# Kernel tuning notes

Measured on AMD Instinct MI355X. Metric: run time of the kernel, lower is better.

The kernel has to match this reference:

```python
import jax, jax.numpy as jnp
import numpy as np

NEG_SLOPE = 0.1  # LeakyReLU alpha from __init__
EPS = 1e-5


def setup_inputs() -> dict:
    key = jax.random.key(0)
    k1, k2, k3, k4, k5 = jax.random.split(key, 5)
    N, E, DIN, DOUT = 10000, 160000, 1024, 1024
    x = jax.random.normal(k1, (N, DIN), dtype=jnp.float32)
    W = jax.random.normal(k2, (DIN, DOUT), dtype=jnp.float32) * 0.02  # xavier-ish gain
    a = jax.random.normal(k3, (1, 2 * DOUT), dtype=jnp.float32) * 0.02
    src = jax.random.randint(k4, (E,), 0, N, dtype=jnp.int64)  # edge rows i
    dst = jax.random.randint(k5, (E,), 0, N, dtype=jnp.int64)  # edge cols j
    return {"x": x, "W": W, "a": a, "src": src, "dst": dst}


def reference(x, W, a, src, dst):
    N = x.shape[0]
    d = W.shape[1]
    h = x @ W                                   # [N, d]
    # a @ cat(h_src, h_dst)^T == (h @ a_l)[src] + (h @ a_r)[dst]
    a_l, a_r = a[0, :d], a[0, d:]
    al = h @ a_l                                # [N]
    ar = h @ a_r                                # [N]
    e = jnp.exp(-jax.nn.leaky_relu(al[src] + ar[dst], negative_slope=NEG_SLOPE))  # [E]
    # sparse rowsum: A @ ones  ->  segment_sum of e over rows
    rowsum = jax.ops.segment_sum(e, src, num_segments=N)          # [N]
    # sparse aggregate: A @ h  (dropout = identity in eval mode)
    h_prime = jax.ops.segment_sum(e[:, None] * h[dst], src, num_segments=N)  # [N, d]
    h_prime = h_prime / (rowsum[:, None] + EPS)
    return jax.nn.elu(h_prime)  # concat=True branch
```

## Files before the change

### kernel.cpp

```cpp
#include <hip/hip_runtime.h>
#include <hip/hip_bf16.h>
#include <stdint.h>
#include <math.h>

#define DK 1024
#define DN 1024
#define CAP 64

typedef __attribute__((ext_vector_type(8))) short bf16x8;
typedef __attribute__((ext_vector_type(4))) float f32x4;
typedef __attribute__((ext_vector_type(8))) unsigned short u16x8;

__device__ __forceinline__ unsigned short f2bf(float f) {
  union { float f; uint32_t u; } v; v.f = f;
  uint32_t r = v.u + 0x7FFFu + ((v.u >> 16) & 1u);
  return (unsigned short)(r >> 16);
}
__device__ __forceinline__ float bf2f(unsigned short b) {
  union { uint32_t u; float f; } v; v.u = ((uint32_t)b) << 16; return v.f;
}

__device__ __forceinline__ void gload_lds16(const void* g, void* l) {
  __builtin_amdgcn_global_load_lds((const __attribute__((address_space(1))) unsigned int*)g,
                                   (__attribute__((address_space(3))) unsigned int*)l,
                                   16, 0, 0);
}

__device__ __forceinline__ void block_reduce2(float& pl, float& pr) {
#pragma unroll
  for (int off = 32; off >= 1; off >>= 1) {
    pl += __shfl_down(pl, off);
    pr += __shfl_down(pr, off);
  }
  __shared__ float sl[4], sr[4];
  int w = threadIdx.x >> 6, lane = threadIdx.x & 63;
  if (lane == 0) { sl[w] = pl; sr[w] = pr; }
  __syncthreads();
  if (threadIdx.x == 0) {
    pl = sl[0] + sl[1] + sl[2] + sl[3];
    pr = sr[0] + sr[1] + sr[2] + sr[3];
  }
}

__global__ __launch_bounds__(256) void wvec_kernel(const float* __restrict__ W,
                                                   const float* __restrict__ a,
                                                   float* __restrict__ wl,
                                                   float* __restrict__ wr,
                                                   int* __restrict__ cnt, int M) {
  int idx = blockIdx.x * 256 + threadIdx.x;
  if (idx < M) cnt[idx] = 0;
  int k = blockIdx.x;
  int tid = threadIdx.x;
  float4 wv = ((const float4*)(W + (size_t)k * DN))[tid];
  float4 l4 = ((const float4*)a)[tid];
  float4 r4 = ((const float4*)(a + DN))[tid];
  float pl = wv.x * l4.x + wv.y * l4.y + wv.z * l4.z + wv.w * l4.w;
  float pr = wv.x * r4.x + wv.y * r4.y + wv.z * r4.z + wv.w * r4.w;
  block_reduce2(pl, pr);
  if (tid == 0) { wl[k] = pl; wr[k] = pr; }
}

__global__ __launch_bounds__(256) void prep_kernel(const float* __restrict__ x,
                                                   unsigned short* __restrict__ xb,
                                                   const float* __restrict__ W,
                                                   unsigned short* __restrict__ Wt,
                                                   const float* __restrict__ wl,
                                                   const float* __restrict__ wr,
                                                   float* __restrict__ al,
                                                   float* __restrict__ ar,
                                                   int M) {
  if ((int)blockIdx.x < M) {
    int row = blockIdx.x;
    int tid = threadIdx.x;
    float4 v = ((const float4*)(x + (size_t)row * DK))[tid];
    ushort4 o;
    o.x = f2bf(v.x); o.y = f2bf(v.y); o.z = f2bf(v.z); o.w = f2bf(v.w);
    ((ushort4*)(xb + (size_t)row * DK))[tid] = o;
    float4 l4 = ((const float4*)wl)[tid];
    float4 r4 = ((const float4*)wr)[tid];
    float pl = v.x * l4.x + v.y * l4.y + v.z * l4.z + v.w * l4.w;
    float pr = v.x * r4.x + v.y * r4.y + v.z * r4.z + v.w * r4.w;
    block_reduce2(pl, pr);
    if (tid == 0) { al[row] = pl; ar[row] = pr; }
  } else {
    __shared__ float t[32][33];
    int bid = blockIdx.x - M;
    int tx = threadIdx.x & 31, ty = threadIdx.x >> 5;
    int bk = (bid & 31) * 32, bn = (bid >> 5) * 32;
#pragma unroll
    for (int rr = 0; rr < 4; ++rr) {
      int row = ty + rr * 8;
      t[row][tx] = W[(size_t)(bk + row) * DN + bn + tx];
    }
    __syncthreads();
#pragma unroll
    for (int rr = 0; rr < 4; ++rr) {
      int row = ty + rr * 8;
      Wt[(size_t)(bn + row) * DK + bk + tx] = f2bf(t[tx][row]);
    }
  }
}

__global__ __launch_bounds__(256) void gemm_kernel(const unsigned short* __restrict__ A,
                                                   const unsigned short* __restrict__ Bt,
                                                   unsigned short* __restrict__ Hb,
                                                   int M) {
  __shared__ unsigned short As[128 * 32];
  __shared__ unsigned short Bs[128 * 32];
  const int tid = threadIdx.x;
  const int w = tid >> 6, lane = tid & 63;
  const int r = lane & 15, q = lane >> 4;
  const int m0 = blockIdx.x * 128, n0 = blockIdx.y * 128;
  const int wr = (w >> 1) * 64, wc = (w & 1) * 64;

  const int c0 = w * 64 + lane;
  const int rowA0 = c0 >> 2, g0 = c0 & 3;
  const int rowA1 = rowA0 + 64;
  int gr0 = m0 + rowA0; if (gr0 >= M) gr0 = M - 1;
  int gr1 = m0 + rowA1; if (gr1 >= M) gr1 = M - 1;
  const unsigned short* gA0 = A + (size_t)gr0 * DK + g0 * 8;
  const unsigned short* gA1 = A + (size_t)gr1 * DK + g0 * 8;
  const unsigned short* gB0 = Bt + (size_t)(n0 + rowA0) * DK + g0 * 8;
  const unsigned short* gB1 = Bt + (size_t)(n0 + rowA1) * DK + g0 * 8;
  unsigned short* lA0 = As + w * 512;
  unsigned short* lA1 = As + 2048 + w * 512;
  unsigned short* lB0 = Bs + w * 512;
  unsigned short* lB1 = Bs + 2048 + w * 512;

  const f32x4 zero = {0.f, 0.f, 0.f, 0.f};
  f32x4 acc[4][4];
#pragma unroll
  for (int i = 0; i < 4; ++i)
#pragma unroll
    for (int j = 0; j < 4; ++j) acc[i][j] = zero;

  for (int k0 = 0; k0 < DK; k0 += 32) {
    gload_lds16(gA0, lA0);
    gload_lds16(gA1, lA1);
    gload_lds16(gB0, lB0);
    gload_lds16(gB1, lB1);
    gA0 += 32; gA1 += 32; gB0 += 32; gB1 += 32;
    __syncthreads();

    bf16x8 af[4], bfr[4];
#pragma unroll
    for (int i = 0; i < 4; ++i)
      af[i] = *(const bf16x8*)&As[(wr + i * 16 + r) * 32 + q * 8];
#pragma unroll
    for (int j = 0; j < 4; ++j)
      bfr[j] = *(const bf16x8*)&Bs[(wc + j * 16 + r) * 32 + q * 8];
#pragma unroll
    for (int i = 0; i < 4; ++i)
#pragma unroll
      for (int j = 0; j < 4; ++j)
        acc[i][j] = __builtin_amdgcn_mfma_f32_16x16x32_bf16(af[i], bfr[j], acc[i][j], 0, 0, 0);
    __syncthreads();
  }

#pragma unroll
  for (int i = 0; i < 4; ++i) {
#pragma unroll
    for (int reg = 0; reg < 4; ++reg) {
      int m = m0 + wr + i * 16 + q * 4 + reg;
      if (m < M) {
#pragma unroll
        for (int j = 0; j < 4; ++j) {
          int n = n0 + wc + j * 16 + r;
          Hb[(size_t)m * DN + n] = f2bf(acc[i][j][reg]);
        }
      }
    }
  }
}

__global__ __launch_bounds__(256) void edge_kernel(const int* __restrict__ src,
                                                   const int* __restrict__ dst,
                                                   const float* __restrict__ al,
                                                   const float* __restrict__ ar,
                                                   int* __restrict__ cnt,
                                                   int* __restrict__ bdst,
                                                   float* __restrict__ be, int E) {
  int i = blockIdx.x * 256 + threadIdx.x;
  if (i < E) {
    int s = src[i], d = dst[i];
    float v = al[s] + ar[d];
    float lr = v > 0.f ? v : 0.1f * v;
    float e = expf(-lr);
    int pos = atomicAdd(&cnt[s], 1);
    if (pos < CAP) {
      bdst[(s << 6) + pos] = d;
      be[(s << 6) + pos] = e;
    }
  }
}

__device__ __forceinline__ void agg_batch16(const int* __restrict__ bdst,
                                            const float* __restrict__ be,
                                            const unsigned short* __restrict__ Hc,
                                            int base, int p, int n,
                                            float (&acc)[8], float& rs) {
  int d[16]; float e[16];
#pragma unroll
  for (int u = 0; u < 4; ++u) {
    int4 d4 = *(const int4*)(bdst + base + p + 4 * u);
    float4 e4 = *(const float4*)(be + base + p + 4 * u);
    d[4 * u + 0] = d4.x; d[4 * u + 1] = d4.y; d[4 * u + 2] = d4.z; d[4 * u + 3] = d4.w;
    e[4 * u + 0] = e4.x; e[4 * u + 1] = e4.y; e[4 * u + 2] = e4.z; e[4 * u + 3] = e4.w;
  }
#pragma unroll
  for (int j = 0; j < 16; ++j) {
    bool valid = (p + j) < n;
    d[j] = valid ? d[j] : 0;
    e[j] = valid ? e[j] : 0.f;
  }
  u16x8 hv[16];
#pragma unroll
  for (int j = 0; j < 16; ++j)
    hv[j] = *(const u16x8*)(Hc + (size_t)d[j] * DN);
#pragma unroll
  for (int j = 0; j < 16; ++j) {
    float ej = e[j];
    rs += ej;
#pragma unroll
    for (int c = 0; c < 8; ++c)
      acc[c] += ej * bf2f(hv[j][c]);
  }
}

__global__ __launch_bounds__(256) void aggregate_kernel(const int* __restrict__ cnt,
                                                        const int* __restrict__ bdst,
                                                        const float* __restrict__ be,
                                                        const unsigned short* __restrict__ Hb,
                                                        float* __restrict__ out, int M) {
  int row = (blockIdx.x << 1) + (threadIdx.x >> 7);
  if (row >= M) return;
  int t = threadIdx.x & 127;
  int n = cnt[row]; if (n > CAP) n = CAP;
  int base = row << 6;
  size_t coff = (size_t)t * 8;
  const unsigned short* Hc = Hb + coff;
  float acc[8] = {0.f, 0.f, 0.f, 0.f, 0.f, 0.f, 0.f, 0.f};
  float rs = 0.f;

  agg_batch16(bdst, be, Hc, base, 0, n, acc, rs);
  if (n > 16)
    agg_batch16(bdst, be, Hc, base, 16, n, acc, rs);
  if (n > 32) {
    for (int p = 32; p < n; ++p) {
      int dd = bdst[base + p];
      float ee = be[base + p];
      rs += ee;
      u16x8 hvv = *(const u16x8*)(Hc + (size_t)dd * DN);
#pragma unroll
      for (int c = 0; c < 8; ++c)
        acc[c] += ee * bf2f(hvv[c]);
    }
  }

  float inv = 1.f / (rs + 1e-5f);
  f32x4 lo, hi;
#pragma unroll
  for (int c = 0; c < 4; ++c) {
    float v = acc[c] * inv;
    lo[c] = v > 0.f ? v : (expf(v) - 1.f);
  }
#pragma unroll
  for (int c = 0; c < 4; ++c) {
    float v = acc[c + 4] * inv;
    hi[c] = v > 0.f ? v : (expf(v) - 1.f);
  }
  f32x4* op = (f32x4*)(out + (size_t)row * DN + coff);
  __builtin_nontemporal_store(lo, op);
  __builtin_nontemporal_store(hi, op + 1);
}

extern "C" void kernel_launch(void* const* d_in, const int* in_sizes, int n_in,
                              void* d_out, int out_size, void* d_ws, size_t ws_size,
                              hipStream_t stream) {
  const float* x = (const float*)d_in[0];
  const float* W = (const float*)d_in[1];
  const float* a = (const float*)d_in[2];
  const int* src = (const int*)d_in[3];
  const int* dst = (const int*)d_in[4];
  float* out = (float*)d_out;
  const int M = in_sizes[0] / DK;
  const int E = in_sizes[3];

  size_t off = 0;
  auto alloc = [&](size_t bytes) -> void* {
    void* p = (char*)d_ws + off;
    off += (bytes + 255) & ~(size_t)255;
    return p;
  };
  unsigned short* xb   = (unsigned short*)alloc((size_t)M * DK * 2);
  unsigned short* Wt   = (unsigned short*)alloc((size_t)DK * DN * 2);
  unsigned short* Hb   = (unsigned short*)alloc((size_t)M * DN * 2);
  float*          al   = (float*)alloc((size_t)M * 4);
  float*          ar   = (float*)alloc((size_t)M * 4);
  float*          wl   = (float*)alloc((size_t)DK * 4);
  float*          wr   = (float*)alloc((size_t)DK * 4);
  int*            cnt  = (int*)alloc((size_t)M * 4);
  int*            bdst = (int*)alloc((size_t)M * CAP * 4);
  float*          be   = (float*)alloc((size_t)M * CAP * 4);

  wvec_kernel<<<DK, 256, 0, stream>>>(W, a, wl, wr, cnt, M);
  prep_kernel<<<M + (DK / 32) * (DN / 32), 256, 0, stream>>>(x, xb, W, Wt, wl, wr, al, ar, M);
  gemm_kernel<<<dim3((M + 127) / 128, DN / 128), 256, 0, stream>>>(xb, Wt, Hb, M);
  edge_kernel<<<(E + 255) / 256, 256, 0, stream>>>(src, dst, al, ar, cnt, bdst, be, E);
  aggregate_kernel<<<(M + 1) / 2, 256, 0, stream>>>(cnt, bdst, be, Hb, out, M);
}
```

Baseline: 194.0 us.

## Double-buffer GEMM LDS tiles to overlap global loads with MFMA

Doubles the shared-memory A/B tiles and prefetches the next K-slice into the alternate buffer while MFMAs run on the current one, dropping one barrier per iteration. This hides global-to-LDS load latency behind compute. It doubles LDS use per block (32KB), which can lower occupancy. Correctness relies on the barrier at the end of each step plus the implicit vmcnt wait before the next reads.

```diff
diff --git a/kernel.cpp b/kernel.cpp
--- a/kernel.cpp
+++ b/kernel.cpp
@@ -105,8 +105,8 @@
                                                    const unsigned short* __restrict__ Bt,
                                                    unsigned short* __restrict__ Hb,
                                                    int M) {
-  __shared__ unsigned short As[128 * 32];
-  __shared__ unsigned short Bs[128 * 32];
+  __shared__ unsigned short As[2][128 * 32];
+  __shared__ unsigned short Bs[2][128 * 32];
   const int tid = threadIdx.x;
   const int w = tid >> 6, lane = tid & 63;
   const int r = lane & 15, q = lane >> 4;
@@ -122,10 +122,8 @@
   const unsigned short* gA1 = A + (size_t)gr1 * DK + g0 * 8;
   const unsigned short* gB0 = Bt + (size_t)(n0 + rowA0) * DK + g0 * 8;
   const unsigned short* gB1 = Bt + (size_t)(n0 + rowA1) * DK + g0 * 8;
-  unsigned short* lA0 = As + w * 512;
-  unsigned short* lA1 = As + 2048 + w * 512;
-  unsigned short* lB0 = Bs + w * 512;
-  unsigned short* lB1 = Bs + 2048 + w * 512;
+  const int l0 = w * 512;
+  const int l1 = 2048 + w * 512;
 
   const f32x4 zero = {0.f, 0.f, 0.f, 0.f};
   f32x4 acc[4][4];
@@ -134,26 +132,39 @@
 #pragma unroll
     for (int j = 0; j < 4; ++j) acc[i][j] = zero;
 
-  for (int k0 = 0; k0 < DK; k0 += 32) {
-    gload_lds16(gA0, lA0);
-    gload_lds16(gA1, lA1);
-    gload_lds16(gB0, lB0);
-    gload_lds16(gB1, lB1);
-    gA0 += 32; gA1 += 32; gB0 += 32; gB1 += 32;
-    __syncthreads();
-
+  gload_lds16(gA0, &As[0][l0]);
+  gload_lds16(gA1, &As[0][l1]);
+  gload_lds16(gB0, &Bs[0][l0]);
+  gload_lds16(gB1, &Bs[0][l1]);
+  gA0 += 32; gA1 += 32; gB0 += 32; gB1 += 32;
+  __syncthreads();
+
+  for (int step = 0; step < 32; ++step) {
+    const int cur = step & 1;
+    if (step < 31) {
+      const int nxt = cur ^ 1;
+      gload_lds16(gA0, &As[nxt][l0]);
+      gload_lds16(gA1, &As[nxt][l1]);
+      gload_lds16(gB0, &Bs[nxt][l0]);
+      gload_lds16(gB1, &Bs[nxt][l1]);
+      gA0 += 32; gA1 += 32; gB0 += 32; gB1 += 32;
+    }
+
+    const unsigned short* Ab = &As[cur][0];
+    const unsigned short* Bb = &Bs[cur][0];
     bf16x8 af[4], bfr[4];
 #pragma unroll
     for (int i = 0; i < 4; ++i)
-      af[i] = *(const bf16x8*)&As[(wr + i * 16 + r) * 32 + q * 8];
+      af[i] = *(const bf16x8*)&Ab[(wr + i * 16 + r) * 32 + q * 8];
 #pragma unroll
     for (int j = 0; j < 4; ++j)
-      bfr[j] = *(const bf16x8*)&Bs[(wc + j * 16 + r) * 32 + q * 8];
+      bfr[j] = *(const bf16x8*)&Bb[(wc + j * 16 + r) * 32 + q * 8];
 #pragma unroll
     for (int i = 0; i < 4; ++i)
 #pragma unroll
       for (int j = 0; j < 4; ++j)
         acc[i][j] = __builtin_amdgcn_mfma_f32_16x16x32_bf16(af[i], bfr[j], acc[i][j], 0, 0, 0);
+
     __syncthreads();
   }
 
```

New measurement: 198.7 us. +2.4%, slower.

## Fuse attention projections into GEMM epilogue and drop wvec kernel

Applied to the files above, without the earlier changes.

The separate W·a precompute kernel and the per-row dot products in the prep kernel are removed. al and ar are now computed in the GEMM epilogue from the fp32 accumulators, using shuffle reductions and atomicAdd into buffers that the prep kernel zeroes. The aggregate kernel is also split into two launches over row halves. This saves one launch and the block reductions, but adds atomics and changes summation order. The split aggregate adds a launch and has no clear benefit.

```diff
diff --git a/kernel.cpp b/kernel.cpp
--- a/kernel.cpp
+++ b/kernel.cpp
@@ -26,49 +26,16 @@
                                    16, 0, 0);
 }
 
-__device__ __forceinline__ void block_reduce2(float& pl, float& pr) {
-#pragma unroll
-  for (int off = 32; off >= 1; off >>= 1) {
-    pl += __shfl_down(pl, off);
-    pr += __shfl_down(pr, off);
-  }
-  __shared__ float sl[4], sr[4];
-  int w = threadIdx.x >> 6, lane = threadIdx.x & 63;
-  if (lane == 0) { sl[w] = pl; sr[w] = pr; }
-  __syncthreads();
-  if (threadIdx.x == 0) {
-    pl = sl[0] + sl[1] + sl[2] + sl[3];
-    pr = sr[0] + sr[1] + sr[2] + sr[3];
-  }
-}
-
-__global__ __launch_bounds__(256) void wvec_kernel(const float* __restrict__ W,
-                                                   const float* __restrict__ a,
-                                                   float* __restrict__ wl,
-                                                   float* __restrict__ wr,
-                                                   int* __restrict__ cnt, int M) {
-  int idx = blockIdx.x * 256 + threadIdx.x;
-  if (idx < M) cnt[idx] = 0;
-  int k = blockIdx.x;
-  int tid = threadIdx.x;
-  float4 wv = ((const float4*)(W + (size_t)k * DN))[tid];
-  float4 l4 = ((const float4*)a)[tid];
-  float4 r4 = ((const float4*)(a + DN))[tid];
-  float pl = wv.x * l4.x + wv.y * l4.y + wv.z * l4.z + wv.w * l4.w;
-  float pr = wv.x * r4.x + wv.y * r4.y + wv.z * r4.z + wv.w * r4.w;
-  block_reduce2(pl, pr);
-  if (tid == 0) { wl[k] = pl; wr[k] = pr; }
-}
-
 __global__ __launch_bounds__(256) void prep_kernel(const float* __restrict__ x,
                                                    unsigned short* __restrict__ xb,
                                                    const float* __restrict__ W,
                                                    unsigned short* __restrict__ Wt,
-                                                   const float* __restrict__ wl,
-                                                   const float* __restrict__ wr,
                                                    float* __restrict__ al,
                                                    float* __restrict__ ar,
+                                                   int* __restrict__ cnt,
                                                    int M) {
+  int g = blockIdx.x * 256 + threadIdx.x;
+  if (g < M) { al[g] = 0.f; ar[g] = 0.f; cnt[g] = 0; }
   if ((int)blockIdx.x < M) {
     int row = blockIdx.x;
     int tid = threadIdx.x;
@@ -76,12 +43,6 @@
     ushort4 o;
     o.x = f2bf(v.x); o.y = f2bf(v.y); o.z = f2bf(v.z); o.w = f2bf(v.w);
     ((ushort4*)(xb + (size_t)row * DK))[tid] = o;
-    float4 l4 = ((const float4*)wl)[tid];
-    float4 r4 = ((const float4*)wr)[tid];
-    float pl = v.x * l4.x + v.y * l4.y + v.z * l4.z + v.w * l4.w;
-    float pr = v.x * r4.x + v.y * r4.y + v.z * r4.z + v.w * r4.w;
-    block_reduce2(pl, pr);
-    if (tid == 0) { al[row] = pl; ar[row] = pr; }
   } else {
     __shared__ float t[32][33];
     int bid = blockIdx.x - M;
@@ -103,7 +64,10 @@
 
 __global__ __launch_bounds__(256) void gemm_kernel(const unsigned short* __restrict__ A,
                                                    const unsigned short* __restrict__ Bt,
+                                                   const float* __restrict__ a,
                                                    unsigned short* __restrict__ Hb,
+                                                   float* __restrict__ al,
+                                                   float* __restrict__ ar,
                                                    int M) {
   __shared__ unsigned short As[128 * 32];
   __shared__ unsigned short Bs[128 * 32];
@@ -168,6 +132,34 @@
           int n = n0 + wc + j * 16 + r;
           Hb[(size_t)m * DN + n] = f2bf(acc[i][j][reg]);
         }
+      }
+    }
+  }
+
+  float alv[4], arv[4];
+#pragma unroll
+  for (int j = 0; j < 4; ++j) {
+    int n = n0 + wc + j * 16 + r;
+    alv[j] = a[n];
+    arv[j] = a[DN + n];
+  }
+#pragma unroll
+  for (int i = 0; i < 4; ++i) {
+#pragma unroll
+    for (int reg = 0; reg < 4; ++reg) {
+      float pl = alv[0] * acc[i][0][reg] + alv[1] * acc[i][1][reg]
+               + alv[2] * acc[i][2][reg] + alv[3] * acc[i][3][reg];
+      float pr = arv[0] * acc[i][0][reg] + arv[1] * acc[i][1][reg]
+               + arv[2] * acc[i][2][reg] + arv[3] * acc[i][3][reg];
+#pragma unroll
+      for (int off = 8; off >= 1; off >>= 1) {
+        pl += __shfl_xor(pl, off);
+        pr += __shfl_xor(pr, off);
+      }
+      int m = m0 + wr + i * 16 + q * 4 + reg;
+      if (r == 0 && m < M) {
+        atomicAdd(al + m, pl);
+        atomicAdd(ar + m, pr);
       }
     }
   }
@@ -231,9 +223,10 @@
                                                         const int* __restrict__ bdst,
                                                         const float* __restrict__ be,
                                                         const unsigned short* __restrict__ Hb,
-                                                        float* __restrict__ out, int M) {
-  int row = (blockIdx.x << 1) + (threadIdx.x >> 7);
-  if (row >= M) return;
+                                                        float* __restrict__ out,
+                                                        int row0, int rowEnd) {
+  int row = row0 + (blockIdx.x << 1) + (threadIdx.x >> 7);
+  if (row >= rowEnd) return;
   int t = threadIdx.x & 127;
   int n = cnt[row]; if (n > CAP) n = CAP;
   int base = row << 6;
@@ -297,15 +290,14 @@
   unsigned short* Hb   = (unsigned short*)alloc((size_t)M * DN * 2);
   float*          al   = (float*)alloc((size_t)M * 4);
   float*          ar   = (float*)alloc((size_t)M * 4);
-  float*          wl   = (float*)alloc((size_t)DK * 4);
-  float*          wr   = (float*)alloc((size_t)DK * 4);
   int*            cnt  = (int*)alloc((size_t)M * 4);
   int*            bdst = (int*)alloc((size_t)M * CAP * 4);
   float*          be   = (float*)alloc((size_t)M * CAP * 4);
 
-  wvec_kernel<<<DK, 256, 0, stream>>>(W, a, wl, wr, cnt, M);
-  prep_kernel<<<M + (DK / 32) * (DN / 32), 256, 0, stream>>>(x, xb, W, Wt, wl, wr, al, ar, M);
-  gemm_kernel<<<dim3((M + 127) / 128, DN / 128), 256, 0, stream>>>(xb, Wt, Hb, M);
+  prep_kernel<<<M + (DK / 32) * (DN / 32), 256, 0, stream>>>(x, xb, W, Wt, al, ar, cnt, M);
+  gemm_kernel<<<dim3((M + 127) / 128, DN / 128), 256, 0, stream>>>(xb, Wt, a, Hb, al, ar, M);
   edge_kernel<<<(E + 255) / 256, 256, 0, stream>>>(src, dst, al, ar, cnt, bdst, be, E);
-  aggregate_kernel<<<(M + 1) / 2, 256, 0, stream>>>(cnt, bdst, be, Hb, out, M);
-}
+  const int Mh = (M + 1) / 2;
+  aggregate_kernel<<<(Mh + 1) / 2, 256, 0, stream>>>(cnt, bdst, be, Hb, out, 0, Mh);
+  aggregate_kernel<<<(M - Mh + 1) / 2, 256, 0, stream>>>(cnt, bdst, be, Hb, out, Mh, M);
+}
```

Result: slower. 216.5 us (+11.6%).
